# Performance work log

Measured on AMD Instinct MI355X. Metric: run time of the kernel, lower is better.

Reference implementation:

```python
import jax, jax.numpy as jnp
import numpy as np

V = 50257   # vocab_size
E = 300     # embedding_dim
H2 = 1024   # hidden_size*2
CH = 6      # char_num
PMR = 32    # pmr_size
SX = 8192   # encoded_x seq len
SC = 4096   # encoded_con seq len
B = 1       # batch (decode step assumes b=1, see argmax/.item() in source)
S = 0.05    # weight init scale


def setup_inputs() -> dict:
    key = jax.random.key(0)
    ks = jax.random.split(key, 20)
    return {
        'input_idx': jax.random.randint(ks[0], (B,), 0, V),
        'encoded_x': jax.random.normal(ks[1], (B, SX, H2), jnp.float32),
        'encoded_con': jax.random.normal(ks[2], (B, SC, H2), jnp.float32),
        'p_matrix': jax.random.normal(ks[3], (B, CH * PMR, H2), jnp.float32),
        'hid': jax.random.normal(ks[4], (1, B, H2), jnp.float32),
        'c': jax.random.normal(ks[5], (1, B, H2), jnp.float32),
        'mask_x': jnp.ones((B, SX), bool),
        'mask_c': jnp.ones((B, SC), bool),
        # learned parameters
        'embed': jax.random.normal(ks[6], (V, E)) * S,
        'Wa': jax.random.normal(ks[7], (2 * H2, H2)) * S,   # Bahdanau attn proj
        'ba': jnp.zeros((H2,)),
        'va': jax.random.normal(ks[8], (H2,)) * S,
        'Wg': jax.random.normal(ks[9], (2 * H2, H2)) * S,   # fc_gate1
        'bg': jnp.zeros((H2,)),
        'Wchar': jax.random.normal(ks[10], (E + 2 * H2, CH)) * S,
        'bchar': jnp.zeros((CH,)),
        'Wp': jax.random.normal(ks[11], (H2, H2)) * S,       # w_p
        'bp': jnp.zeros((H2,)),
        'Wh': jax.random.normal(ks[12], (H2, H2)) * S,       # w_h
        'bh': jnp.zeros((H2,)),
        'vv': jax.random.normal(ks[13], (H2,)) * S,          # v (no bias)
        'Wy': jax.random.normal(ks[14], (E + 2 * H2, E)) * S,  # y_inp
        'by': jnp.zeros((E,)),
        'Wih': jax.random.normal(ks[15], (E, 4 * H2)) * S,   # LSTM input weights (i,f,g,o)
        'Whh': jax.random.normal(ks[16], (H2, 4 * H2)) * S,
        'bih': jnp.zeros((4 * H2,)),
        'bhh': jnp.zeros((4 * H2,)),
        'Wout': jax.random.normal(ks[17], (H2, V)) * S,      # out2
        'bout': jnp.zeros((V,)),
    }


def reference(input_idx, encoded_x, encoded_con, p_matrix, hid, c, mask_x, mask_c,
              embed, Wa, ba, va, Wg, bg, Wchar, bchar, Wp, bp, Wh, bh, vv,
              Wy, by, Wih, Whh, bih, bhh, Wout, bout):
    b = input_idx.shape[0]
    h0 = hid[0]                    # [b, 2h]
    c0 = c[0]
    y_input = embed[input_idx]     # [b, e] (dropout is identity at eval)

    def bahdanau(h, enc, mask):
        # h: [b,2h], enc: [b,seq,2h], mask: [b,seq] -> softmax weights [b,seq]
        hrep = jnp.broadcast_to(h[:, None, :], enc.shape)
        energy = jnp.tanh(jnp.concatenate([hrep, enc], -1) @ Wa + ba)  # [b,seq,2h]
        scores = energy @ va                                          # [b,seq]
        scores = jnp.where(mask, scores, -1e10)
        return jax.nn.softmax(scores, axis=1)

    a_x = bahdanau(h0, encoded_x, mask_x)
    weighted_x = jnp.einsum('bs,bsd->bd', a_x, encoded_x)
    a_c = bahdanau(h0, encoded_con, mask_c)
    weighted_c = jnp.einsum('bs,bsd->bd', a_c, encoded_con)
    weighted = jnp.concatenate([weighted_x, weighted_c], -1) @ Wg + bg  # [b,2h]

    # pointer: soft gate over chars -> hard one-hot selection -> gather rows of p_matrix
    g_char = jax.nn.softmax(jnp.concatenate([y_input, h0, weighted], -1) @ Wchar + bchar, axis=1)  # [b,6]
    pm = p_matrix.reshape(b, CH, -1)                       # [b,6,pmr*2h]
    nz = (pm.sum(axis=2) != 0).astype(g_char.dtype)
    z_char = g_char * nz
    o_char = jax.nn.one_hot(jnp.argmax(z_char, axis=1), CH, dtype=z_char.dtype)  # [b,6]
    s_char = (o_char[:, :, None] * pm).reshape(b, CH * PMR, H2)                  # [b,192,2h]

    # additive attention over the 192 selected slots (replicates source repeat/view layout, valid for b=1)
    hh = jnp.tile(h0, (CH * PMR, 1))                       # [192*b, 2h]
    pp = (s_char @ Wp + bp).reshape(-1, H2)                # [b*192, 2h]
    att = jnp.tanh(hh @ Wh + bh + pp) @ vv                 # [192*b]
    p_attn_score = jax.nn.softmax(att.reshape(b, -1), axis=1)     # [b,192]
    p_attn = jnp.einsum('bn,bnd->bd', p_attn_score, s_char)       # [b,2h]
    ps6 = p_attn_score.reshape(CH, -1)                            # [6, b*32]
    sel = jnp.argmax(o_char.reshape(-1))
    p_attn_score_sel = jnp.take(ps6, sel, axis=0)[None, :]        # [1, b*32]

    # LSTM cell step (torch gate order i,f,g,o)
    y_in = jnp.concatenate([y_input, weighted, p_attn], -1) @ Wy + by  # [b,e]
    gates = y_in @ Wih + bih + h0 @ Whh + bhh                          # [b,8h]
    gi, gf, gg, go = jnp.split(gates, 4, axis=1)
    c1 = jax.nn.sigmoid(gf) * c0 + jax.nn.sigmoid(gi) * jnp.tanh(gg)
    h1 = jax.nn.sigmoid(go) * jnp.tanh(c1)

    out = jax.nn.softmax(h1 @ Wout + bout, axis=1)[:, None, :]  # [b,1,vocab]
    return (out, h1[None], c1[None], weighted[:, None, :], p_attn_score_sel)
```

## Files before the change

### kernel.cpp

```cpp
#include <hip/hip_runtime.h>
#include <hip/hip_bf16.h>
#include <math.h>

typedef short short8 __attribute__((ext_vector_type(8)));
typedef float f32x4 __attribute__((ext_vector_type(4)));
typedef float f32x4u __attribute__((ext_vector_type(4), aligned(4)));

#define DEV static __device__ __forceinline__

DEV void gl2lds16(const void* g, void* l) {
  __builtin_amdgcn_global_load_lds(
      (const __attribute__((address_space(1))) unsigned int*)g,
      (__attribute__((address_space(3))) unsigned int*)l, 16, 0, 0);
}

DEV float wred_sum(float v) {
#pragma unroll
  for (int o = 1; o < 64; o <<= 1) v += __shfl_xor(v, o, 64);
  return v;
}
DEV float wred_max(float v) {
#pragma unroll
  for (int o = 1; o < 64; o <<= 1) v = fmaxf(v, __shfl_xor(v, o, 64));
  return v;
}
DEV float sigmoidf(float x) { return 1.0f / (1.0f + expf(-x)); }

DEV unsigned short f2bf(float x) {
  unsigned u = __float_as_uint(x);
  unsigned rr = (u + 0x7fffu + ((u >> 16) & 1u)) >> 16;
  return (unsigned short)rr;
}

DEV short8 cvt8(float4 f0, float4 f1) {
  union { short8 s; unsigned u[4]; } r;
  asm("v_cvt_pk_bf16_f32 %0, %1, %2" : "=v"(r.u[0]) : "v"(f0.x), "v"(f0.y));
  asm("v_cvt_pk_bf16_f32 %0, %1, %2" : "=v"(r.u[1]) : "v"(f0.z), "v"(f0.w));
  asm("v_cvt_pk_bf16_f32 %0, %1, %2" : "=v"(r.u[2]) : "v"(f1.x), "v"(f1.y));
  asm("v_cvt_pk_bf16_f32 %0, %1, %2" : "=v"(r.u[3]) : "v"(f1.z), "v"(f1.w));
  return r.s;
}

#define OUT_H1 50257
#define OUT_C1 51281
#define OUT_W  52305
#define OUT_PS 53329
#define PKS 50260

__global__ void k_prep(const float* __restrict__ ex, const float* __restrict__ ec,
                       const float* __restrict__ Wa, const float* __restrict__ ba,
                       const float* __restrict__ Wh, const float* __restrict__ bh,
                       const float* __restrict__ hid, const float* __restrict__ embed,
                       const int* __restrict__ idx, const float* __restrict__ pmat,
                       unsigned short* __restrict__ encb, unsigned short* __restrict__ WaT,
                       float* __restrict__ hWa, float* __restrict__ hWh,
                       float* __restrict__ yinp, float* __restrict__ nz) {
  int bx = blockIdx.x, t = threadIdx.x;
  if (bx < 6144) {
    size_t i = ((size_t)bx * 256 + t) * 8;
    const float* src = (i < 8388608) ? (ex + i) : (ec + (i - 8388608));
    float4 f0 = *(const float4*)src;
    float4 f1 = *(const float4*)(src + 4);
    *(short8*)&encb[i] = cvt8(f0, f1);
  } else if (bx < 6400) {
    __shared__ float tile[64][65];
    int bb = bx - 6144;
    int bi = bb >> 4, bj = bb & 15;
    int c = t & 63, rq = t >> 6;
#pragma unroll
    for (int rr = 0; rr < 16; rr++) {
      int kl = rr * 4 + rq;
      tile[kl][c] = Wa[(size_t)(1024 + bi * 64 + kl) * 1024 + bj * 64 + c];
    }
    __syncthreads();
#pragma unroll
    for (int rr = 0; rr < 16; rr++) {
      int nl = rr * 4 + rq;
      WaT[(size_t)(bj * 64 + nl) * 1024 + bi * 64 + c] = f2bf(tile[c][nl]);
    }
  } else if (bx < 6432) {
    __shared__ float red[4][64];
    int bb = bx - 6400;
    int ol = t & 63, kc = t >> 6;
    int o = bb * 64 + ol;
    const float* W = (o < 1024) ? Wa : Wh;
    int col = (o < 1024) ? o : (o - 1024);
    float acc = 0.f;
#pragma unroll 4
    for (int k = kc * 256; k < kc * 256 + 256; k++) acc += hid[k] * W[(size_t)k * 1024 + col];
    red[kc][ol] = acc;
    __syncthreads();
    if (t < 64) {
      int oo = bb * 64 + t;
      float s = red[0][t] + red[1][t] + red[2][t] + red[3][t];
      if (oo < 1024) hWa[oo] = s + ba[oo];
      else hWh[oo - 1024] = s + bh[oo - 1024];
    }
  } else if (bx == 6432) {
    int id = idx[0];
    for (int k = t; k < 300; k += 256) yinp[k] = embed[(size_t)id * 300 + k];
  } else {
    __shared__ float r2[4];
    int j = bx - 6433;
    float a = 0.f;
    for (int k = t; k < 32768; k += 256) a += pmat[(size_t)j * 32768 + k];
    a = wred_sum(a);
    if ((t & 63) == 0) r2[t >> 6] = a;
    __syncthreads();
    if (t == 0) nz[j] = r2[0] + r2[1] + r2[2] + r2[3];
  }
}

__global__ __launch_bounds__(256, 2) void k_scores_gemm(
    const unsigned short* __restrict__ encb, const unsigned short* __restrict__ WaT,
    const float* __restrict__ hWa, const float* __restrict__ va,
    float* __restrict__ scoresP) {
  __shared__ __align__(16) unsigned short As[128 * 64];
  __shared__ __align__(16) unsigned short Bs[256 * 64];
  __shared__ float red[2][128];
  int mtile = blockIdx.x, ntile = blockIdx.y;
  int t = threadIdx.x, lane = t & 63, wid = t >> 6;
  int wr = wid >> 1, wc = wid & 1;
  int l15 = lane & 15, lg = lane >> 4;
  int r0 = mtile * 128;

  f32x4 acc[4][8];
#pragma unroll
  for (int m = 0; m < 4; m++)
#pragma unroll
    for (int n = 0; n < 8; n++) acc[m][n] = (f32x4){0.f, 0.f, 0.f, 0.f};

  for (int kt = 0; kt < 1024; kt += 64) {
#pragma unroll
    for (int p = 0; p < 4; p++) {
      int c = p * 256 + t;
      int row = c >> 3, slot = c & 7;
      const unsigned short* g =
          encb + (size_t)(r0 + row) * 1024 + kt + ((slot ^ (row & 7)) * 8);
      gl2lds16(g, &As[c * 8]);
    }
#pragma unroll
    for (int p = 0; p < 8; p++) {
      int c = p * 256 + t;
      int row = c >> 3, slot = c & 7;
      const unsigned short* g =
          WaT + (size_t)(ntile * 256 + row) * 1024 + kt + ((slot ^ (row & 7)) * 8);
      gl2lds16(g, &Bs[c * 8]);
    }
    __syncthreads();
#pragma unroll
    for (int ks = 0; ks < 2; ks++) {
      int q = ks * 4 + lg;
      short8 a[4];
#pragma unroll
      for (int m = 0; m < 4; m++) {
        int row = wr * 64 + m * 16 + l15;
        a[m] = *(const short8*)&As[row * 64 + ((q ^ (row & 7)) * 8)];
      }
#pragma unroll
      for (int n = 0; n < 8; n++) {
        int nr = wc * 128 + n * 16 + l15;
        short8 b = *(const short8*)&Bs[nr * 64 + ((q ^ (nr & 7)) * 8)];
#pragma unroll
        for (int m = 0; m < 4; m++)
          acc[m][n] = __builtin_amdgcn_mfma_f32_16x16x32_bf16(a[m], b, acc[m][n], 0, 0, 0);
      }
    }
    __syncthreads();
  }

  float vva[8], hba[8];
#pragma unroll
  for (int n = 0; n < 8; n++) {
    int col = ntile * 256 + wc * 128 + n * 16 + l15;
    vva[n] = va[col];
    hba[n] = hWa[col];
  }
#pragma unroll
  for (int m = 0; m < 4; m++) {
#pragma unroll
    for (int j = 0; j < 4; j++) {
      float p = 0.f;
#pragma unroll
      for (int n = 0; n < 8; n++) p += vva[n] * tanhf(acc[m][n][j] + hba[n]);
#pragma unroll
      for (int o = 1; o < 16; o <<= 1) p += __shfl_xor(p, o, 64);
      if (l15 == 0) red[wc][wr * 64 + m * 16 + lg * 4 + j] = p;
    }
  }
  __syncthreads();
  if (t < 128) scoresP[(size_t)ntile * 12288 + r0 + t] = red[0][t] + red[1][t];
}

__global__ void k_scores_reduce(const float* __restrict__ scoresP, float* __restrict__ scores,
                                float* __restrict__ bmax, float* __restrict__ bz) {
  __shared__ float r4[4];
  int bx = blockIdx.x, t = threadIdx.x;
  int r = bx * 256 + t;
  float s = 0.f;
#pragma unroll
  for (int nt = 0; nt < 4; nt++) s += scoresP[(size_t)nt * 12288 + r];
  scores[r] = s;
  float m = wred_max(s);
  if ((t & 63) == 0) r4[t >> 6] = m;
  __syncthreads();
  m = fmaxf(fmaxf(r4[0], r4[1]), fmaxf(r4[2], r4[3]));
  __syncthreads();
  float z = expf(s - m);
  z = wred_sum(z);
  if ((t & 63) == 0) r4[t >> 6] = z;
  __syncthreads();
  if (t == 0) { bmax[bx] = m; bz[bx] = r4[0] + r4[1] + r4[2] + r4[3]; }
}

__global__ void k_weighted_part(const unsigned short* __restrict__ encb,
                                const float* __restrict__ scores, const float* __restrict__ bmax,
                                const float* __restrict__ bz, float* __restrict__ partw) {
  __shared__ float wrow[64];
  int b = blockIdx.x, colq = blockIdx.y, t = threadIdx.x;
  int seg = (b >= 128) ? 1 : 0;
  int sbase = seg ? 8192 : 0;
  int rb = seg ? (b - 128) * 64 : b * 64;
  if (t < 64) {
    int b0 = seg ? 32 : 0, cnt = seg ? 16 : 32;
    float mv = (t < cnt) ? bmax[b0 + t] : -1e30f;
    float m = wred_max(mv);
    float zv = (t < cnt) ? bz[b0 + t] * expf(bmax[b0 + t] - m) : 0.f;
    float z = wred_sum(zv);
    wrow[t] = expf(scores[sbase + rb + t] - m) / z;
  }
  __syncthreads();
  int c2 = colq * 512 + 2 * t;
  float a0 = 0.f, a1 = 0.f;
  size_t rowbase = (size_t)b * 64 * 1024;
#pragma unroll 8
  for (int r = 0; r < 64; r++) {
    unsigned u = *(const unsigned*)&encb[rowbase + (size_t)r * 1024 + c2];
    float w = wrow[r];
    a0 += w * __uint_as_float(u << 16);
    a1 += w * __uint_as_float(u & 0xffff0000u);
  }
  float2 o; o.x = a0; o.y = a1;
  *(float2*)&partw[(size_t)b * 1024 + c2] = o;
}

__global__ void k_weighted_gemv(const float* __restrict__ partw, const float* __restrict__ Wg,
                                float* __restrict__ wgP) {
  __shared__ float wxcL[64];
  int oq = blockIdx.x, kq = blockIdx.y, t = threadIdx.x;
  if (t < 64) {
    float s = 0.f;
    if (kq < 16) {
      int d = kq * 64 + t;
#pragma unroll 8
      for (int b = 0; b < 128; b++) s += partw[(size_t)b * 1024 + d];
    } else {
      int d = (kq - 16) * 64 + t;
#pragma unroll 8
      for (int b = 128; b < 192; b++) s += partw[(size_t)b * 1024 + d];
    }
    wxcL[t] = s;
  }
  __syncthreads();
  int o = oq * 256 + t;
  int k0 = kq * 64;
  float acc = 0.f;
#pragma unroll 8
  for (int j = 0; j < 64; j++) acc += wxcL[j] * Wg[(size_t)(k0 + j) * 1024 + o];
  wgP[(size_t)kq * 1024 + o] = acc;
}

__global__ void k_wgfin_charsel(const float* __restrict__ wgP, const float* __restrict__ bg,
                                const float* __restrict__ yinp, const float* __restrict__ hid,
                                const float* __restrict__ Wchar, const float* __restrict__ bchar,
                                const float* __restrict__ nz, float* __restrict__ weighted,
                                int* __restrict__ sel, float* __restrict__ dout) {
  __shared__ float WL[1024];
  __shared__ float red[4][6];
  int t = threadIdx.x;
  for (int q = 0; q < 4; q++) {
    int d = t + q * 256;
    float s = bg[d];
#pragma unroll 8
    for (int b = 0; b < 32; b++) s += wgP[(size_t)b * 1024 + d];
    WL[d] = s;
    weighted[d] = s;
    dout[OUT_W + d] = s;
  }
  __syncthreads();
  float p[6] = {0.f, 0.f, 0.f, 0.f, 0.f, 0.f};
  for (int k = t; k < 2348; k += 256) {
    float xv = (k < 300) ? yinp[k] : (k < 1324 ? hid[k - 300] : WL[k - 1324]);
#pragma unroll
    for (int ch = 0; ch < 6; ch++) p[ch] += xv * Wchar[k * 6 + ch];
  }
#pragma unroll
  for (int ch = 0; ch < 6; ch++) {
    float v = wred_sum(p[ch]);
    if ((t & 63) == 0) red[t >> 6][ch] = v;
  }
  __syncthreads();
  if (t == 0) {
    float best = -1e30f; int si = 0;
    for (int ch = 0; ch < 6; ch++) {
      float lgt = red[0][ch] + red[1][ch] + red[2][ch] + red[3][ch] + bchar[ch];
      if (nz[ch] != 0.0f && lgt > best) { best = lgt; si = ch; }
    }
    *sel = si;
  }
}

__global__ void k_pp(const float* __restrict__ pmat, const float* __restrict__ Wp,
                     const int* __restrict__ sel, float* __restrict__ ppP) {
  __shared__ float sr[32][64];
  int oq = blockIdx.x, kq = blockIdx.y, t = threadIdx.x;
  int row0 = (*sel) * 32;
  int k0 = kq * 64;
#pragma unroll
  for (int j = 0; j < 8; j++) {
    int idx = t + j * 256;
    int i = idx >> 6, kk = idx & 63;
    sr[i][kk] = pmat[(size_t)(row0 + i) * 1024 + k0 + kk];
  }
  __syncthreads();
  int o = oq * 256 + t;
  float acc[32];
#pragma unroll
  for (int i = 0; i < 32; i++) acc[i] = 0.f;
  for (int k = 0; k < 64; k++) {
    float w = Wp[(size_t)(k0 + k) * 1024 + o];
#pragma unroll
    for (int i = 0; i < 32; i++) acc[i] += sr[i][k] * w;
  }
#pragma unroll
  for (int i = 0; i < 32; i++) ppP[(size_t)kq * 32768 + i * 1024 + o] = acc[i];
}

__global__ void k_ppfin_att(const float* __restrict__ ppP, const float* __restrict__ bp,
                            const float* __restrict__ hWh, const float* __restrict__ vv,
                            float* __restrict__ attb) {
  __shared__ float r4[4];
  int i = blockIdx.x, t = threadIdx.x;
  float pt = 0.f;
  if (i < 32) {
    for (int q = 0; q < 4; q++) {
      int d = t + q * 256;
      float s = bp[d];
#pragma unroll
      for (int kq = 0; kq < 16; kq++) s += ppP[(size_t)kq * 32768 + i * 1024 + d];
      pt += vv[d] * tanhf(hWh[d] + s);
    }
  } else {
    for (int q = 0; q < 4; q++) {
      int d = t + q * 256;
      pt += vv[d] * tanhf(hWh[d] + bp[d]);
    }
  }
  pt = wred_sum(pt);
  if ((t & 63) == 0) r4[t >> 6] = pt;
  __syncthreads();
  if (t == 0) attb[i] = r4[0] + r4[1] + r4[2] + r4[3];
}

__global__ void k_pattn_yin(const float* __restrict__ attb, const float* __restrict__ pmat,
                            const int* __restrict__ sel, const float* __restrict__ yinp,
                            const float* __restrict__ weighted, const float* __restrict__ Wy,
                            float* __restrict__ yinP, float* __restrict__ dout) {
  __shared__ float sc32[32];
  __shared__ float XLb[74];
  int b = blockIdx.x, t = threadIdx.x;
  if (t == 0) {
    float az = attb[32];
    float m = az;
#pragma unroll
    for (int i = 0; i < 32; i++) m = fmaxf(m, attb[i]);
    float Z = 160.0f * expf(az - m);
#pragma unroll
    for (int i = 0; i < 32; i++) Z += expf(attb[i] - m);
#pragma unroll
    for (int i = 0; i < 32; i++) sc32[i] = expf(attb[i] - m) / Z;
  }
  __syncthreads();
  if (b == 0 && t < 32) dout[OUT_PS + t] = sc32[t];
  int base = b * 74;
  int len = 2348 - base; if (len > 74) len = 74;
  int srow0 = (*sel) * 32;
  if (t < len) {
    int k = base + t;
    float xv;
    if (k < 300) xv = yinp[k];
    else if (k < 1324) xv = weighted[k - 300];
    else {
      int d = k - 1324;
      float acc = 0.f;
#pragma unroll
      for (int i = 0; i < 32; i++) acc += sc32[i] * pmat[(size_t)(srow0 + i) * 1024 + d];
      xv = acc;
    }
    XLb[t] = xv;
  }
  __syncthreads();
  if (t < 300) {
    float acc = 0.f;
    for (int j = 0; j < len; j++) acc += XLb[j] * Wy[(size_t)(base + j) * 300 + t];
    yinP[b * 300 + t] = acc;
  }
}

__global__ void k_gates_part(const float* __restrict__ yinP, const float* __restrict__ by,
                             const float* __restrict__ hid,
                             const float* __restrict__ Wih, const float* __restrict__ Whh,
                             float* __restrict__ gatesP) {
  __shared__ float YLb[40];
  __shared__ float red[4][64];
  int bx = blockIdx.x, kq = blockIdx.y, t = threadIdx.x;
  int k0i = kq * 38;
  int k1i = k0i + 38; if (k1i > 300) k1i = 300;
  if (t < k1i - k0i) {
    float s = by[k0i + t];
#pragma unroll 8
    for (int b = 0; b < 32; b++) s += yinP[b * 300 + k0i + t];
    YLb[t] = s;
  }
  __syncthreads();
  int ol = t & 63, kc = t >> 6;
  int o = bx * 64 + ol;
  float acc = 0.f;
  for (int k = k0i + kc; k < k1i; k += 4) acc += YLb[k - k0i] * Wih[(size_t)k * 4096 + o];
  int kh0 = kq * 128;
#pragma unroll 4
  for (int k = kh0 + kc; k < kh0 + 128; k += 4) acc += hid[k] * Whh[(size_t)k * 4096 + o];
  red[kc][ol] = acc;
  __syncthreads();
  if (t < 64) {
    int oo = bx * 64 + t;
    gatesP[(size_t)kq * 4096 + oo] = red[0][t] + red[1][t] + red[2][t] + red[3][t];
  }
}

__global__ __launch_bounds__(256) void k_out_gemv(const float* __restrict__ gatesP,
                                                  const float* __restrict__ bih,
                                                  const float* __restrict__ bhh,
                                                  const float* __restrict__ c0,
                                                  const float* __restrict__ Wout,
                                                  float* __restrict__ partK,
                                                  float* __restrict__ dout) {
  __shared__ float hh[32];
  int ks = blockIdx.x, cb = blockIdx.y, t = threadIdx.x;
  if (t < 32) {
    int d = ks * 32 + t;
    float gi = bih[d] + bhh[d];
    float gf = bih[1024 + d] + bhh[1024 + d];
    float gg = bih[2048 + d] + bhh[2048 + d];
    float go = bih[3072 + d] + bhh[3072 + d];
#pragma unroll
    for (int kq = 0; kq < 8; kq++) {
      const float* g = gatesP + (size_t)kq * 4096;
      gi += g[d]; gf += g[1024 + d]; gg += g[2048 + d]; go += g[3072 + d];
    }
    float c1 = sigmoidf(gf) * c0[d] + sigmoidf(gi) * tanhf(gg);
    float h1 = sigmoidf(go) * tanhf(c1);
    hh[t] = h1;
    if (cb == 0) { dout[OUT_H1 + d] = h1; dout[OUT_C1 + d] = c1; }
  }
  __syncthreads();
  const float* W = Wout + (size_t)ks * 32 * 50257;
  int c4 = cb * 1024 + t * 4;
  if (c4 + 4 <= 50257) {
    f32x4 a = (f32x4){0.f, 0.f, 0.f, 0.f};
#pragma unroll 4
    for (int k = 0; k < 32; k++) {
      f32x4u w = *(const f32x4u*)&W[(size_t)k * 50257 + c4];
      float h = hh[k];
      a[0] += h * w[0]; a[1] += h * w[1]; a[2] += h * w[2]; a[3] += h * w[3];
    }
    *(f32x4*)&partK[(size_t)ks * PKS + c4] = a;
  } else if (c4 < 50257) {
    for (int c = c4; c < 50257; c++) {
      float a = 0.f;
#pragma unroll 8
      for (int k = 0; k < 32; k++) a += hh[k] * W[(size_t)k * 50257 + c];
      partK[(size_t)ks * PKS + c] = a;
    }
  }
}

__global__ void k_logits_stats(const float* __restrict__ partK, const float* __restrict__ bout,
                               float* __restrict__ logits, float* __restrict__ bstat) {
  __shared__ float r4[4];
  int bx = blockIdx.x, t = threadIdx.x;
  int c = bx * 256 + t;
  float v = -1e30f;
  if (c < 50257) {
    v = bout[c];
#pragma unroll
    for (int ks = 0; ks < 32; ks++) v += partK[(size_t)ks * PKS + c];
    logits[c] = v;
  }
  float m = wred_max(v);
  if ((t & 63) == 0) r4[t >> 6] = m;
  __syncthreads();
  m = fmaxf(fmaxf(r4[0], r4[1]), fmaxf(r4[2], r4[3]));
  __syncthreads();
  float z = (c < 50257) ? expf(v - m) : 0.f;
  z = wred_sum(z);
  if ((t & 63) == 0) r4[t >> 6] = z;
  __syncthreads();
  if (t == 0) { bstat[bx] = m; bstat[256 + bx] = r4[0] + r4[1] + r4[2] + r4[3]; }
}

__global__ void k_out_final(const float* __restrict__ bstat, const float* __restrict__ logits,
                            float* __restrict__ dout) {
  __shared__ float r4m[4], r4z[4];
  int bx = blockIdx.x, t = threadIdx.x;
  float mv = (t < 197) ? bstat[t] : -1e30f;
  float m = wred_max(mv);
  if ((t & 63) == 0) r4m[t >> 6] = m;
  __syncthreads();
  m = fmaxf(fmaxf(r4m[0], r4m[1]), fmaxf(r4m[2], r4m[3]));
  __syncthreads();
  float zv = (t < 197) ? bstat[256 + t] * expf(bstat[t] - m) : 0.f;
  float z = wred_sum(zv);
  if ((t & 63) == 0) r4z[t >> 6] = z;
  __syncthreads();
  float Z = r4z[0] + r4z[1] + r4z[2] + r4z[3];
  int c = bx * 256 + t;
  if (c < 50257) dout[c] = expf(logits[c] - m) / Z;
}

extern "C" void kernel_launch(void* const* d_in, const int* in_sizes, int n_in,
                              void* d_out, int out_size, void* d_ws, size_t ws_size,
                              hipStream_t stream) {
  (void)in_sizes; (void)n_in; (void)out_size; (void)ws_size;
  const int*   idx   = (const int*)  d_in[0];
  const float* ex    = (const float*)d_in[1];
  const float* ec    = (const float*)d_in[2];
  const float* pmat  = (const float*)d_in[3];
  const float* hid   = (const float*)d_in[4];
  const float* c0    = (const float*)d_in[5];
  const float* embed = (const float*)d_in[8];
  const float* Wa    = (const float*)d_in[9];
  const float* ba    = (const float*)d_in[10];
  const float* va    = (const float*)d_in[11];
  const float* Wg    = (const float*)d_in[12];
  const float* bg    = (const float*)d_in[13];
  const float* Wchar = (const float*)d_in[14];
  const float* bchar = (const float*)d_in[15];
  const float* Wp    = (const float*)d_in[16];
  const float* bp    = (const float*)d_in[17];
  const float* Wh    = (const float*)d_in[18];
  const float* bh    = (const float*)d_in[19];
  const float* vv    = (const float*)d_in[20];
  const float* Wy    = (const float*)d_in[21];
  const float* by    = (const float*)d_in[22];
  const float* Wih   = (const float*)d_in[23];
  const float* Whh   = (const float*)d_in[24];
  const float* bih   = (const float*)d_in[25];
  const float* bhh   = (const float*)d_in[26];
  const float* Wout  = (const float*)d_in[27];
  const float* bout  = (const float*)d_in[28];
  float* out = (float*)d_out;

  char* ws = (char*)d_ws;
  unsigned short* encb = (unsigned short*)(ws + 0);
  unsigned short* WaT  = (unsigned short*)(ws + 25165824);
  float* scoresP  = (float*)(ws + 27262976);
  float* scores   = (float*)(ws + 27656192);
  float* bmax     = (float*)(ws + 27705344);
  float* bz       = (float*)(ws + 27705600);
  float* partw    = (float*)(ws + 27705856);
  float* wgP      = (float*)(ws + 28492288);
  float* partK    = (float*)(ws + 0);
  float* logits   = (float*)(ws + 6433280);
  float* ppP      = (float*)(ws + 28623360);
  float* attb     = (float*)(ws + 30720512);
  float* yinP     = (float*)(ws + 30720768);
  float* gatesP   = (float*)(ws + 30759424);
  float* hWa      = (float*)(ws + 30890496);
  float* hWh      = (float*)(ws + 30894592);
  float* yinp     = (float*)(ws + 30898688);
  float* nz       = (float*)(ws + 30900224);
  float* weighted = (float*)(ws + 30900480);
  int*   sel      = (int*)  (ws + 30904576);
  float* bstat    = (float*)(ws + 30904832);

  k_prep<<<6439, 256, 0, stream>>>(ex, ec, Wa, ba, Wh, bh, hid, embed, idx, pmat,
                                   encb, WaT, hWa, hWh, yinp, nz);
  k_scores_gemm<<<dim3(96, 4), 256, 0, stream>>>(encb, WaT, hWa, va, scoresP);
  k_scores_reduce<<<48, 256, 0, stream>>>(scoresP, scores, bmax, bz);
  k_weighted_part<<<dim3(192, 2), 256, 0, stream>>>(encb, scores, bmax, bz, partw);
  k_weighted_gemv<<<dim3(4, 32), 256, 0, stream>>>(partw, Wg, wgP);
  k_wgfin_charsel<<<1, 256, 0, stream>>>(wgP, bg, yinp, hid, Wchar, bchar, nz, weighted, sel, out);
  k_pp<<<dim3(4, 16), 256, 0, stream>>>(pmat, Wp, sel, ppP);
  k_ppfin_att<<<33, 256, 0, stream>>>(ppP, bp, hWh, vv, attb);
  k_pattn_yin<<<32, 320, 0, stream>>>(attb, pmat, sel, yinp, weighted, Wy, yinP, out);
  k_gates_part<<<dim3(64, 8), 256, 0, stream>>>(yinP, by, hid, Wih, Whh, gatesP);
  k_out_gemv<<<dim3(32, 50), 256, 0, stream>>>(gatesP, bih, bhh, c0, Wout, partK, out);
  k_logits_stats<<<197, 256, 0, stream>>>(partK, bout, logits, bstat);
  k_out_final<<<197, 256, 0, stream>>>(bstat, logits, out);
}
```

Measured before the change: 252.2 us.

## Fuse mid-pipeline kernels into one persistent kernel with grid barriers

```diff
diff --git a/kernel.cpp b/kernel.cpp
--- a/kernel.cpp
+++ b/kernel.cpp
@@ -41,6 +41,22 @@
   return r.s;
 }
 
+DEV void gbar(int* cnt, int* gen, int nblk) {
+  __syncthreads();
+  if (threadIdx.x == 0) {
+    int g = __hip_atomic_load(gen, __ATOMIC_RELAXED, __HIP_MEMORY_SCOPE_AGENT);
+    int prev = __hip_atomic_fetch_add(cnt, 1, __ATOMIC_ACQ_REL, __HIP_MEMORY_SCOPE_AGENT);
+    if (prev == nblk - 1) {
+      __hip_atomic_store(cnt, 0, __ATOMIC_RELAXED, __HIP_MEMORY_SCOPE_AGENT);
+      __hip_atomic_store(gen, g + 1, __ATOMIC_RELEASE, __HIP_MEMORY_SCOPE_AGENT);
+    } else {
+      while (__hip_atomic_load(gen, __ATOMIC_ACQUIRE, __HIP_MEMORY_SCOPE_AGENT) == g)
+        __builtin_amdgcn_s_sleep(2);
+    }
+  }
+  __syncthreads();
+}
+
 #define OUT_H1 50257
 #define OUT_C1 51281
 #define OUT_W  52305
@@ -54,7 +70,8 @@
                        const int* __restrict__ idx, const float* __restrict__ pmat,
                        unsigned short* __restrict__ encb, unsigned short* __restrict__ WaT,
                        float* __restrict__ hWa, float* __restrict__ hWh,
-                       float* __restrict__ yinp, float* __restrict__ nz) {
+                       float* __restrict__ yinp, float* __restrict__ nz,
+                       int* __restrict__ barr) {
   int bx = blockIdx.x, t = threadIdx.x;
   if (bx < 6144) {
     size_t i = ((size_t)bx * 256 + t) * 8;
@@ -97,6 +114,7 @@
       else hWh[oo - 1024] = s + bh[oo - 1024];
     }
   } else if (bx == 6432) {
+    if (t < 4) barr[t] = 0;
     int id = idx[0];
     for (int k = t; k < 300; k += 256) yinp[k] = embed[(size_t)id * 300 + k];
   } else {
@@ -192,249 +210,264 @@
   if (t < 128) scoresP[(size_t)ntile * 12288 + r0 + t] = red[0][t] + red[1][t];
 }
 
-__global__ void k_scores_reduce(const float* __restrict__ scoresP, float* __restrict__ scores,
-                                float* __restrict__ bmax, float* __restrict__ bz) {
-  __shared__ float r4[4];
-  int bx = blockIdx.x, t = threadIdx.x;
-  int r = bx * 256 + t;
-  float s = 0.f;
-#pragma unroll
-  for (int nt = 0; nt < 4; nt++) s += scoresP[(size_t)nt * 12288 + r];
-  scores[r] = s;
-  float m = wred_max(s);
-  if ((t & 63) == 0) r4[t >> 6] = m;
-  __syncthreads();
-  m = fmaxf(fmaxf(r4[0], r4[1]), fmaxf(r4[2], r4[3]));
-  __syncthreads();
-  float z = expf(s - m);
-  z = wred_sum(z);
-  if ((t & 63) == 0) r4[t >> 6] = z;
-  __syncthreads();
-  if (t == 0) { bmax[bx] = m; bz[bx] = r4[0] + r4[1] + r4[2] + r4[3]; }
-}
-
-__global__ void k_weighted_part(const unsigned short* __restrict__ encb,
-                                const float* __restrict__ scores, const float* __restrict__ bmax,
-                                const float* __restrict__ bz, float* __restrict__ partw) {
-  __shared__ float wrow[64];
-  int b = blockIdx.x, colq = blockIdx.y, t = threadIdx.x;
-  int seg = (b >= 128) ? 1 : 0;
-  int sbase = seg ? 8192 : 0;
-  int rb = seg ? (b - 128) * 64 : b * 64;
-  if (t < 64) {
-    int b0 = seg ? 32 : 0, cnt = seg ? 16 : 32;
-    float mv = (t < cnt) ? bmax[b0 + t] : -1e30f;
-    float m = wred_max(mv);
-    float zv = (t < cnt) ? bz[b0 + t] * expf(bmax[b0 + t] - m) : 0.f;
-    float z = wred_sum(zv);
-    wrow[t] = expf(scores[sbase + rb + t] - m) / z;
-  }
-  __syncthreads();
-  int c2 = colq * 512 + 2 * t;
-  float a0 = 0.f, a1 = 0.f;
-  size_t rowbase = (size_t)b * 64 * 1024;
+__global__ __launch_bounds__(256) void k_mid(
+    const float* __restrict__ scoresP, float* __restrict__ scores,
+    float* __restrict__ bmax, float* __restrict__ bz,
+    const unsigned short* __restrict__ encb, float* __restrict__ partw,
+    const float* __restrict__ Wg, float* __restrict__ wgP, const float* __restrict__ bg,
+    const float* __restrict__ yinp, const float* __restrict__ hid,
+    const float* __restrict__ Wchar, const float* __restrict__ bchar,
+    const float* __restrict__ nz, float* __restrict__ weighted, int* __restrict__ sel,
+    const float* __restrict__ pmat, const float* __restrict__ Wp, float* __restrict__ ppP,
+    const float* __restrict__ bp, const float* __restrict__ hWh, const float* __restrict__ vv,
+    float* __restrict__ attb, const float* __restrict__ Wy, float* __restrict__ yinP,
+    const float* __restrict__ by, const float* __restrict__ Wih, const float* __restrict__ Whh,
+    float* __restrict__ gatesP, float* __restrict__ dout, int* __restrict__ barr) {
+  int bid = blockIdx.x, t = threadIdx.x;
+  int* cnt = barr; int* gen = barr + 1;
+
+  if (bid < 48) {
+    __shared__ float r4[4];
+    int r = bid * 256 + t;
+    float s = 0.f;
+#pragma unroll
+    for (int nt = 0; nt < 4; nt++) s += scoresP[(size_t)nt * 12288 + r];
+    scores[r] = s;
+    float m = wred_max(s);
+    if ((t & 63) == 0) r4[t >> 6] = m;
+    __syncthreads();
+    m = fmaxf(fmaxf(r4[0], r4[1]), fmaxf(r4[2], r4[3]));
+    __syncthreads();
+    float z = expf(s - m);
+    z = wred_sum(z);
+    if ((t & 63) == 0) r4[t >> 6] = z;
+    __syncthreads();
+    if (t == 0) { bmax[bid] = m; bz[bid] = r4[0] + r4[1] + r4[2] + r4[3]; }
+  }
+  gbar(cnt, gen, 256);
+
+  {
+    __shared__ float wrow[64];
+#pragma unroll
+    for (int pass = 0; pass < 2; pass++) {
+      int u = bid + pass * 256;
+      if (u >= 384) break;
+      int b = u >> 1, colq = u & 1;
+      int seg = (b >= 128) ? 1 : 0;
+      int sbase = seg ? 8192 : 0;
+      int rb = seg ? (b - 128) * 64 : b * 64;
+      if (t < 64) {
+        int b0 = seg ? 32 : 0, cntn = seg ? 16 : 32;
+        float mv = (t < cntn) ? bmax[b0 + t] : -1e30f;
+        float m = wred_max(mv);
+        float zv = (t < cntn) ? bz[b0 + t] * expf(bmax[b0 + t] - m) : 0.f;
+        float z = wred_sum(zv);
+        wrow[t] = expf(scores[sbase + rb + t] - m) / z;
+      }
+      __syncthreads();
+      int c2 = colq * 512 + 2 * t;
+      float a0 = 0.f, a1 = 0.f;
+      size_t rowbase = (size_t)b * 64 * 1024;
 #pragma unroll 8
-  for (int r = 0; r < 64; r++) {
-    unsigned u = *(const unsigned*)&encb[rowbase + (size_t)r * 1024 + c2];
-    float w = wrow[r];
-    a0 += w * __uint_as_float(u << 16);
-    a1 += w * __uint_as_float(u & 0xffff0000u);
-  }
-  float2 o; o.x = a0; o.y = a1;
-  *(float2*)&partw[(size_t)b * 1024 + c2] = o;
-}
-
-__global__ void k_weighted_gemv(const float* __restrict__ partw, const float* __restrict__ Wg,
-                                float* __restrict__ wgP) {
-  __shared__ float wxcL[64];
-  int oq = blockIdx.x, kq = blockIdx.y, t = threadIdx.x;
-  if (t < 64) {
-    float s = 0.f;
-    if (kq < 16) {
-      int d = kq * 64 + t;
+      for (int r = 0; r < 64; r++) {
+        unsigned uu = *(const unsigned*)&encb[rowbase + (size_t)r * 1024 + c2];
+        float w = wrow[r];
+        a0 += w * __uint_as_float(uu << 16);
+        a1 += w * __uint_as_float(uu & 0xffff0000u);
+      }
+      float2 o; o.x = a0; o.y = a1;
+      *(float2*)&partw[(size_t)b * 1024 + c2] = o;
+      __syncthreads();
+    }
+  }
+  gbar(cnt, gen, 256);
+
+  if (bid < 128) {
+    __shared__ float wxcL[64];
+    int oq = bid >> 5, kq = bid & 31;
+    if (t < 64) {
+      float s = 0.f;
+      if (kq < 16) {
+        int d = kq * 64 + t;
 #pragma unroll 8
-      for (int b = 0; b < 128; b++) s += partw[(size_t)b * 1024 + d];
-    } else {
-      int d = (kq - 16) * 64 + t;
+        for (int b = 0; b < 128; b++) s += partw[(size_t)b * 1024 + d];
+      } else {
+        int d = (kq - 16) * 64 + t;
 #pragma unroll 8
-      for (int b = 128; b < 192; b++) s += partw[(size_t)b * 1024 + d];
-    }
-    wxcL[t] = s;
-  }
-  __syncthreads();
-  int o = oq * 256 + t;
-  int k0 = kq * 64;
-  float acc = 0.f;
+        for (int b = 128; b < 192; b++) s += partw[(size_t)b * 1024 + d];
+      }
+      wxcL[t] = s;
+    }
+    __syncthreads();
+    int o = oq * 256 + t;
+    int k0 = kq * 64;
+    float acc = 0.f;
 #pragma unroll 8
-  for (int j = 0; j < 64; j++) acc += wxcL[j] * Wg[(size_t)(k0 + j) * 1024 + o];
-  wgP[(size_t)kq * 1024 + o] = acc;
-}
-
-__global__ void k_wgfin_charsel(const float* __restrict__ wgP, const float* __restrict__ bg,
-                                const float* __restrict__ yinp, const float* __restrict__ hid,
-                                const float* __restrict__ Wchar, const float* __restrict__ bchar,
-                                const float* __restrict__ nz, float* __restrict__ weighted,
-                                int* __restrict__ sel, float* __restrict__ dout) {
-  __shared__ float WL[1024];
-  __shared__ float red[4][6];
-  int t = threadIdx.x;
-  for (int q = 0; q < 4; q++) {
-    int d = t + q * 256;
-    float s = bg[d];
-#pragma unroll 8
-    for (int b = 0; b < 32; b++) s += wgP[(size_t)b * 1024 + d];
-    WL[d] = s;
-    weighted[d] = s;
-    dout[OUT_W + d] = s;
-  }
-  __syncthreads();
-  float p[6] = {0.f, 0.f, 0.f, 0.f, 0.f, 0.f};
-  for (int k = t; k < 2348; k += 256) {
-    float xv = (k < 300) ? yinp[k] : (k < 1324 ? hid[k - 300] : WL[k - 1324]);
-#pragma unroll
-    for (int ch = 0; ch < 6; ch++) p[ch] += xv * Wchar[k * 6 + ch];
-  }
-#pragma unroll
-  for (int ch = 0; ch < 6; ch++) {
-    float v = wred_sum(p[ch]);
-    if ((t & 63) == 0) red[t >> 6][ch] = v;
-  }
-  __syncthreads();
-  if (t == 0) {
-    float best = -1e30f; int si = 0;
-    for (int ch = 0; ch < 6; ch++) {
-      float lgt = red[0][ch] + red[1][ch] + red[2][ch] + red[3][ch] + bchar[ch];
-      if (nz[ch] != 0.0f && lgt > best) { best = lgt; si = ch; }
-    }
-    *sel = si;
-  }
-}
-
-__global__ void k_pp(const float* __restrict__ pmat, const float* __restrict__ Wp,
-                     const int* __restrict__ sel, float* __restrict__ ppP) {
-  __shared__ float sr[32][64];
-  int oq = blockIdx.x, kq = blockIdx.y, t = threadIdx.x;
-  int row0 = (*sel) * 32;
-  int k0 = kq * 64;
-#pragma unroll
-  for (int j = 0; j < 8; j++) {
-    int idx = t + j * 256;
-    int i = idx >> 6, kk = idx & 63;
-    sr[i][kk] = pmat[(size_t)(row0 + i) * 1024 + k0 + kk];
-  }
-  __syncthreads();
-  int o = oq * 256 + t;
-  float acc[32];
-#pragma unroll
-  for (int i = 0; i < 32; i++) acc[i] = 0.f;
-  for (int k = 0; k < 64; k++) {
-    float w = Wp[(size_t)(k0 + k) * 1024 + o];
-#pragma unroll
-    for (int i = 0; i < 32; i++) acc[i] += sr[i][k] * w;
-  }
-#pragma unroll
-  for (int i = 0; i < 32; i++) ppP[(size_t)kq * 32768 + i * 1024 + o] = acc[i];
-}
-
-__global__ void k_ppfin_att(const float* __restrict__ ppP, const float* __restrict__ bp,
-                            const float* __restrict__ hWh, const float* __restrict__ vv,
-                            float* __restrict__ attb) {
-  __shared__ float r4[4];
-  int i = blockIdx.x, t = threadIdx.x;
-  float pt = 0.f;
-  if (i < 32) {
+    for (int j = 0; j < 64; j++) acc += wxcL[j] * Wg[(size_t)(k0 + j) * 1024 + o];
+    wgP[(size_t)kq * 1024 + o] = acc;
+  }
+  gbar(cnt, gen, 256);
+
+  if (bid == 0) {
+    __shared__ float WL[1024];
+    __shared__ float red6[4][6];
     for (int q = 0; q < 4; q++) {
       int d = t + q * 256;
-      float s = bp[d];
-#pragma unroll
-      for (int kq = 0; kq < 16; kq++) s += ppP[(size_t)kq * 32768 + i * 1024 + d];
-      pt += vv[d] * tanhf(hWh[d] + s);
-    }
-  } else {
-    for (int q = 0; q < 4; q++) {
-      int d = t + q * 256;
-      pt += vv[d] * tanhf(hWh[d] + bp[d]);
-    }
-  }
-  pt = wred_sum(pt);
-  if ((t & 63) == 0) r4[t >> 6] = pt;
-  __syncthreads();
-  if (t == 0) attb[i] = r4[0] + r4[1] + r4[2] + r4[3];
-}
-
-__global__ void k_pattn_yin(const float* __restrict__ attb, const float* __restrict__ pmat,
-                            const int* __restrict__ sel, const float* __restrict__ yinp,
-                            const float* __restrict__ weighted, const float* __restrict__ Wy,
-                            float* __restrict__ yinP, float* __restrict__ dout) {
-  __shared__ float sc32[32];
-  __shared__ float XLb[74];
-  int b = blockIdx.x, t = threadIdx.x;
-  if (t == 0) {
-    float az = attb[32];
-    float m = az;
-#pragma unroll
-    for (int i = 0; i < 32; i++) m = fmaxf(m, attb[i]);
-    float Z = 160.0f * expf(az - m);
-#pragma unroll
-    for (int i = 0; i < 32; i++) Z += expf(attb[i] - m);
-#pragma unroll
-    for (int i = 0; i < 32; i++) sc32[i] = expf(attb[i] - m) / Z;
-  }
-  __syncthreads();
-  if (b == 0 && t < 32) dout[OUT_PS + t] = sc32[t];
-  int base = b * 74;
-  int len = 2348 - base; if (len > 74) len = 74;
-  int srow0 = (*sel) * 32;
-  if (t < len) {
-    int k = base + t;
-    float xv;
-    if (k < 300) xv = yinp[k];
-    else if (k < 1324) xv = weighted[k - 300];
-    else {
-      int d = k - 1324;
+      float s = bg[d];
+#pragma unroll 8
+      for (int b = 0; b < 32; b++) s += wgP[(size_t)b * 1024 + d];
+      WL[d] = s;
+      weighted[d] = s;
+      dout[OUT_W + d] = s;
+    }
+    __syncthreads();
+    float p[6] = {0.f, 0.f, 0.f, 0.f, 0.f, 0.f};
+    for (int k = t; k < 2348; k += 256) {
+      float xv = (k < 300) ? yinp[k] : (k < 1324 ? hid[k - 300] : WL[k - 1324]);
+#pragma unroll
+      for (int ch = 0; ch < 6; ch++) p[ch] += xv * Wchar[k * 6 + ch];
+    }
+#pragma unroll
+    for (int ch = 0; ch < 6; ch++) {
+      float v = wred_sum(p[ch]);
+      if ((t & 63) == 0) red6[t >> 6][ch] = v;
+    }
+    __syncthreads();
+    if (t == 0) {
+      float best = -1e30f; int si = 0;
+      for (int ch = 0; ch < 6; ch++) {
+        float lgt = red6[0][ch] + red6[1][ch] + red6[2][ch] + red6[3][ch] + bchar[ch];
+        if (nz[ch] != 0.0f && lgt > best) { best = lgt; si = ch; }
+      }
+      *sel = si;
+    }
+  }
+  gbar(cnt, gen, 256);
+
+  if (bid < 64) {
+    __shared__ float sr[32][64];
+    int oq = bid >> 4, kq = bid & 15;
+    int row0 = (*sel) * 32;
+    int k0 = kq * 64;
+#pragma unroll
+    for (int j = 0; j < 8; j++) {
+      int idx2 = t + j * 256;
+      int i = idx2 >> 6, kk = idx2 & 63;
+      sr[i][kk] = pmat[(size_t)(row0 + i) * 1024 + k0 + kk];
+    }
+    __syncthreads();
+    int o = oq * 256 + t;
+    float acc[32];
+#pragma unroll
+    for (int i = 0; i < 32; i++) acc[i] = 0.f;
+    for (int k = 0; k < 64; k++) {
+      float w = Wp[(size_t)(k0 + k) * 1024 + o];
+#pragma unroll
+      for (int i = 0; i < 32; i++) acc[i] += sr[i][k] * w;
+    }
+#pragma unroll
+    for (int i = 0; i < 32; i++) ppP[(size_t)kq * 32768 + i * 1024 + o] = acc[i];
+  }
+  gbar(cnt, gen, 256);
+
+  if (bid < 33) {
+    __shared__ float r4b[4];
+    int i = bid;
+    float pt = 0.f;
+    if (i < 32) {
+      for (int q = 0; q < 4; q++) {
+        int d = t + q * 256;
+        float s = bp[d];
+#pragma unroll
+        for (int kq = 0; kq < 16; kq++) s += ppP[(size_t)kq * 32768 + i * 1024 + d];
+        pt += vv[d] * tanhf(hWh[d] + s);
+      }
+    } else {
+      for (int q = 0; q < 4; q++) {
+        int d = t + q * 256;
+        pt += vv[d] * tanhf(hWh[d] + bp[d]);
+      }
+    }
+    pt = wred_sum(pt);
+    if ((t & 63) == 0) r4b[t >> 6] = pt;
+    __syncthreads();
+    if (t == 0) attb[i] = r4b[0] + r4b[1] + r4b[2] + r4b[3];
+  }
+  gbar(cnt, gen, 256);
+
+  if (bid < 32) {
+    __shared__ float sc32[32];
+    __shared__ float XLb[74];
+    if (t == 0) {
+      float az = attb[32];
+      float m = az;
+#pragma unroll
+      for (int i = 0; i < 32; i++) m = fmaxf(m, attb[i]);
+      float Z = 160.0f * expf(az - m);
+#pragma unroll
+      for (int i = 0; i < 32; i++) Z += expf(attb[i] - m);
+#pragma unroll
+      for (int i = 0; i < 32; i++) sc32[i] = expf(attb[i] - m) / Z;
+    }
+    __syncthreads();
+    if (bid == 0 && t < 32) dout[OUT_PS + t] = sc32[t];
+    int base = bid * 74;
+    int len = 2348 - base; if (len > 74) len = 74;
+    int srow0 = (*sel) * 32;
+    if (t < len) {
+      int k = base + t;
+      float xv;
+      if (k < 300) xv = yinp[k];
+      else if (k < 1324) xv = weighted[k - 300];
+      else {
+        int d = k - 1324;
+        float acc = 0.f;
+#pragma unroll
+        for (int i = 0; i < 32; i++) acc += sc32[i] * pmat[(size_t)(srow0 + i) * 1024 + d];
+        xv = acc;
+      }
+      XLb[t] = xv;
+    }
+    __syncthreads();
+    for (int o = t; o < 300; o += 256) {
       float acc = 0.f;
-#pragma unroll
-      for (int i = 0; i < 32; i++) acc += sc32[i] * pmat[(size_t)(srow0 + i) * 1024 + d];
-      xv = acc;
-    }
-    XLb[t] = xv;
-  }
-  __syncthreads();
-  if (t < 300) {
-    float acc = 0.f;
-    for (int j = 0; j < len; j++) acc += XLb[j] * Wy[(size_t)(base + j) * 300 + t];
-    yinP[b * 300 + t] = acc;
-  }
-}
-
-__global__ void k_gates_part(const float* __restrict__ yinP, const float* __restrict__ by,
-                             const float* __restrict__ hid,
-                             const float* __restrict__ Wih, const float* __restrict__ Whh,
-                             float* __restrict__ gatesP) {
-  __shared__ float YLb[40];
-  __shared__ float red[4][64];
-  int bx = blockIdx.x, kq = blockIdx.y, t = threadIdx.x;
-  int k0i = kq * 38;
-  int k1i = k0i + 38; if (k1i > 300) k1i = 300;
-  if (t < k1i - k0i) {
-    float s = by[k0i + t];
+      for (int j = 0; j < len; j++) acc += XLb[j] * Wy[(size_t)(base + j) * 300 + o];
+      yinP[bid * 300 + o] = acc;
+    }
+  }
+  gbar(cnt, gen, 256);
+
+  {
+    __shared__ float YLb[40];
+    __shared__ float red8[4][64];
+#pragma unroll
+    for (int pass = 0; pass < 2; pass++) {
+      int u = bid + pass * 256;
+      int bx = u >> 3, kq = u & 7;
+      int k0i = kq * 38;
+      int k1i = k0i + 38; if (k1i > 300) k1i = 300;
+      if (t < k1i - k0i) {
+        float s = by[k0i + t];
 #pragma unroll 8
-    for (int b = 0; b < 32; b++) s += yinP[b * 300 + k0i + t];
-    YLb[t] = s;
-  }
-  __syncthreads();
-  int ol = t & 63, kc = t >> 6;
-  int o = bx * 64 + ol;
-  float acc = 0.f;
-  for (int k = k0i + kc; k < k1i; k += 4) acc += YLb[k - k0i] * Wih[(size_t)k * 4096 + o];
-  int kh0 = kq * 128;
+        for (int b = 0; b < 32; b++) s += yinP[b * 300 + k0i + t];
+        YLb[t] = s;
+      }
+      __syncthreads();
+      int ol = t & 63, kc = t >> 6;
+      int o = bx * 64 + ol;
+      float acc = 0.f;
+      for (int k = k0i + kc; k < k1i; k += 4) acc += YLb[k - k0i] * Wih[(size_t)k * 4096 + o];
+      int kh0 = kq * 128;
 #pragma unroll 4
-  for (int k = kh0 + kc; k < kh0 + 128; k += 4) acc += hid[k] * Whh[(size_t)k * 4096 + o];
-  red[kc][ol] = acc;
-  __syncthreads();
-  if (t < 64) {
-    int oo = bx * 64 + t;
-    gatesP[(size_t)kq * 4096 + oo] = red[0][t] + red[1][t] + red[2][t] + red[3][t];
+      for (int k = kh0 + kc; k < kh0 + 128; k += 4) acc += hid[k] * Whh[(size_t)k * 4096 + o];
+      red8[kc][ol] = acc;
+      __syncthreads();
+      if (t < 64) {
+        int oo = bx * 64 + t;
+        gatesP[(size_t)kq * 4096 + oo] = red8[0][t] + red8[1][t] + red8[2][t] + red8[3][t];
+      }
+      __syncthreads();
+    }
   }
 }
 
@@ -485,9 +518,14 @@
   }
 }
 
-__global__ void k_logits_stats(const float* __restrict__ partK, const float* __restrict__ bout,
-                               float* __restrict__ logits, float* __restrict__ bstat) {
+__global__ __launch_bounds__(256) void k_logits_fin(const float* __restrict__ partK,
+                                                    const float* __restrict__ bout,
+                                                    float* __restrict__ logits,
+                                                    float* __restrict__ bstat,
+                                                    float* __restrict__ dout,
+                                                    int* __restrict__ barr) {
   __shared__ float r4[4];
+  __shared__ float r4z[4];
   int bx = blockIdx.x, t = threadIdx.x;
   int c = bx * 256 + t;
   float v = -1e30f;
@@ -507,25 +545,21 @@
   if ((t & 63) == 0) r4[t >> 6] = z;
   __syncthreads();
   if (t == 0) { bstat[bx] = m; bstat[256 + bx] = r4[0] + r4[1] + r4[2] + r4[3]; }
-}
-
-__global__ void k_out_final(const float* __restrict__ bstat, const float* __restrict__ logits,
-                            float* __restrict__ dout) {
-  __shared__ float r4m[4], r4z[4];
-  int bx = blockIdx.x, t = threadIdx.x;
+
+  gbar(barr + 2, barr + 3, 197);
+
   float mv = (t < 197) ? bstat[t] : -1e30f;
-  float m = wred_max(mv);
-  if ((t & 63) == 0) r4m[t >> 6] = m;
-  __syncthreads();
-  m = fmaxf(fmaxf(r4m[0], r4m[1]), fmaxf(r4m[2], r4m[3]));
-  __syncthreads();
-  float zv = (t < 197) ? bstat[256 + t] * expf(bstat[t] - m) : 0.f;
-  float z = wred_sum(zv);
-  if ((t & 63) == 0) r4z[t >> 6] = z;
+  float gm = wred_max(mv);
+  if ((t & 63) == 0) r4[t >> 6] = gm;
+  __syncthreads();
+  gm = fmaxf(fmaxf(r4[0], r4[1]), fmaxf(r4[2], r4[3]));
+  __syncthreads();
+  float zv = (t < 197) ? bstat[256 + t] * expf(bstat[t] - gm) : 0.f;
+  float gz = wred_sum(zv);
+  if ((t & 63) == 0) r4z[t >> 6] = gz;
   __syncthreads();
   float Z = r4z[0] + r4z[1] + r4z[2] + r4z[3];
-  int c = bx * 256 + t;
-  if (c < 50257) dout[c] = expf(logits[c] - m) / Z;
+  if (c < 50257) dout[c] = expf(logits[c] - gm) / Z;
 }
 
 extern "C" void kernel_launch(void* const* d_in, const int* in_sizes, int n_in,
@@ -583,19 +617,15 @@
   float* weighted = (float*)(ws + 30900480);
   int*   sel      = (int*)  (ws + 30904576);
   float* bstat    = (float*)(ws + 30904832);
+  int*   barr     = (int*)  (ws + 30906880);
 
   k_prep<<<6439, 256, 0, stream>>>(ex, ec, Wa, ba, Wh, bh, hid, embed, idx, pmat,
-                                   encb, WaT, hWa, hWh, yinp, nz);
+                                   encb, WaT, hWa, hWh, yinp, nz, barr);
   k_scores_gemm<<<dim3(96, 4), 256, 0, stream>>>(encb, WaT, hWa, va, scoresP);
-  k_scores_reduce<<<48, 256, 0, stream>>>(scoresP, scores, bmax, bz);
-  k_weighted_part<<<dim3(192, 2), 256, 0, stream>>>(encb, scores, bmax, bz, partw);
-  k_weighted_gemv<<<dim3(4, 32), 256, 0, stream>>>(partw, Wg, wgP);
-  k_wgfin_charsel<<<1, 256, 0, stream>>>(wgP, bg, yinp, hid, Wchar, bchar, nz, weighted, sel, out);
-  k_pp<<<dim3(4, 16), 256, 0, stream>>>(pmat, Wp, sel, ppP);
-  k_ppfin_att<<<33, 256, 0, stream>>>(ppP, bp, hWh, vv, attb);
-  k_pattn_yin<<<32, 320, 0, stream>>>(attb, pmat, sel, yinp, weighted, Wy, yinP, out);
-  k_gates_part<<<dim3(64, 8), 256, 0, stream>>>(yinP, by, hid, Wih, Whh, gatesP);
+  k_mid<<<256, 256, 0, stream>>>(scoresP, scores, bmax, bz, encb, partw, Wg, wgP, bg,
+                                 yinp, hid, Wchar, bchar, nz, weighted, sel, pmat, Wp,
+                                 ppP, bp, hWh, vv, attb, Wy, yinP, by, Wih, Whh,
+                                 gatesP, out, barr);
   k_out_gemv<<<dim3(32, 50), 256, 0, stream>>>(gatesP, bih, bhh, c0, Wout, partK, out);
-  k_logits_stats<<<197, 256, 0, stream>>>(partK, bout, logits, bstat);
-  k_out_final<<<197, 256, 0, stream>>>(bstat, logits, out);
-}
+  k_logits_fin<<<197, 256, 0, stream>>>(partK, bout, logits, bstat, out, barr);
+}
```

Result: slower. 549.0 us (+117.7%).
